# Performance work log

Hardware: AMD Instinct MI355X
Metric: run time of the kernel (lower is better)

## Reference

```python
import jax, jax.numpy as jnp
import numpy as np
import math

B, T, D_MODEL, N_HEADS = 4, 2048, 1024, 16
D_HEAD = D_MODEL // N_HEADS


def _rope_freqs(t, d_head):
    inv = 1.0 / (10000.0 ** (np.arange(0, d_head, 2, dtype=np.float32) / d_head))
    ang = np.arange(t, dtype=np.float32)[:, None] * inv[None, :]  # (T, d_head//2)
    return jnp.asarray(np.cos(ang)), jnp.asarray(np.sin(ang))


def setup_inputs() -> dict:
    key = jax.random.key(0)
    k1, k2, k3, k4, k5 = jax.random.split(key, 5)
    s = 1.0 / math.sqrt(D_MODEL)
    x = jax.random.normal(k1, (B, T, D_MODEL), dtype=jnp.float32)
    mask = jnp.triu(jnp.ones((T, T), dtype=bool), k=1)  # causal: mask future positions
    freqs_cos, freqs_sin = _rope_freqs(T, D_HEAD)
    qkv_w = jax.random.uniform(k2, (3 * D_MODEL, D_MODEL), jnp.float32, -s, s)
    qkv_b = jax.random.uniform(k3, (3 * D_MODEL,), jnp.float32, -s, s)
    proj_w = jax.random.uniform(k4, (D_MODEL, D_MODEL), jnp.float32, -s, s)
    proj_b = jax.random.uniform(k5, (D_MODEL,), jnp.float32, -s, s)
    return {"x": x, "mask": mask, "freqs_cos": freqs_cos, "freqs_sin": freqs_sin,
            "qkv_w": qkv_w, "qkv_b": qkv_b, "proj_w": proj_w, "proj_b": proj_b}


def _apply_rope(t, cos, sin):
    # t: (B, H, T, D_HEAD); cos/sin: (T, D_HEAD//2), broadcast over B, H
    tp = t.reshape(*t.shape[:-1], -1, 2)
    a, b = tp[..., 0], tp[..., 1]
    out_r = a * cos - b * sin
    out_i = a * sin + b * cos
    return jnp.stack([out_r, out_i], axis=-1).reshape(t.shape)


def reference(x, mask, freqs_cos, freqs_sin, qkv_w, qkv_b, proj_w, proj_b):
    Bx, Tx, C = x.shape
    qkv = x @ qkv_w.T + qkv_b  # (B, T, 3C)
    q, k, v = jnp.split(qkv, 3, axis=-1)
    def heads(z):
        return z.reshape(Bx, Tx, N_HEADS, D_HEAD).transpose(0, 2, 1, 3)  # (B,H,T,dh)
    q, k, v = heads(q), heads(k), heads(v)
    q = _apply_rope(q, freqs_cos, freqs_sin)
    k = _apply_rope(k, freqs_cos, freqs_sin)
    att = jnp.einsum('bhqd,bhkd->bhqk', q, k) / math.sqrt(D_HEAD)
    att = jnp.where(mask, -jnp.inf, att)
    att = jax.nn.softmax(att, axis=-1)
    out = jnp.einsum('bhqk,bhkd->bhqd', att, v)
    out = out.transpose(0, 2, 1, 3).reshape(Bx, Tx, C)
    return out @ proj_w.T + proj_b
```

## Files before the change

### kernel.cpp

```cpp
#include <hip/hip_runtime.h>
#include <stdint.h>

#define BB 4
#define TT 2048
#define CC 1024
#define HH 16
#define DH 64
#define NQKV 3072

typedef __bf16 bf16_t;
typedef __attribute__((ext_vector_type(8))) __bf16 bf16x8;
typedef __attribute__((ext_vector_type(4))) float f32x4;

#define MFMA16(a, b, c) __builtin_amdgcn_mfma_f32_16x16x32_bf16((a), (b), (c), 0, 0, 0)

__device__ __forceinline__ void gll16(const void* g, void* l) {
  typedef const __attribute__((address_space(1))) void* gp_t;
  typedef __attribute__((address_space(3))) void* lp_t;
  __builtin_amdgcn_global_load_lds((gp_t)(uintptr_t)g, (lp_t)(uintptr_t)l, 16, 0, 0);
}

__global__ __launch_bounds__(256) void cvt_k(const float* __restrict__ src,
                                             bf16_t* __restrict__ dst, int n) {
  const int i8 = (blockIdx.x * 256 + threadIdx.x) * 8;
  if (i8 < n) {
    const f32x4 a = *(const f32x4*)(src + i8);
    const f32x4 b = *(const f32x4*)(src + i8 + 4);
    bf16x8 r;
    r[0] = (bf16_t)a[0]; r[1] = (bf16_t)a[1]; r[2] = (bf16_t)a[2]; r[3] = (bf16_t)a[3];
    r[4] = (bf16_t)b[0]; r[5] = (bf16_t)b[1]; r[6] = (bf16_t)b[2]; r[7] = (bf16_t)b[3];
    *(bf16x8*)(dst + i8) = r;
  }
}

template <int EPI>
__global__ __launch_bounds__(512, 2) void gemm_k(
    const bf16_t* __restrict__ A, const bf16_t* __restrict__ W,
    const float* __restrict__ bias,
    const float* __restrict__ fcos, const float* __restrict__ fsin,
    void* __restrict__ out0v, bf16_t* __restrict__ out1,
    bf16_t* __restrict__ out2) {
  __shared__ bf16_t Al[2][16384];
  __shared__ bf16_t Bl[2][16384];
  const int K = 1024;
  const int tid = threadIdx.x;
  const int lane = tid & 63, wave = tid >> 6;
  const int quad = lane >> 4, c = lane & 15;
  const int wm = wave >> 2, wn = wave & 3;
  const int mbase = blockIdx.y * 256, nbase = blockIdx.x * 256;

  f32x4 acc[8][4];
#pragma unroll
  for (int i = 0; i < 8; ++i)
#pragma unroll
    for (int j = 0; j < 4; ++j) acc[i][j] = (f32x4){0.f, 0.f, 0.f, 0.f};

  const int r0 = tid >> 3;
  const int cc0 = (tid & 7) ^ (r0 & 7);
  const bf16_t* Ag = A + (size_t)(mbase + r0) * K + cc0 * 8;
  const bf16_t* Bg = W + (size_t)(nbase + r0) * K + cc0 * 8;
  const int ls0 = tid * 8, ls1 = ls0 + 4096, ls2 = ls0 + 8192, ls3 = ls0 + 12288;

  const int rbA = (wm * 128 + c) * 64;
  const int rbB = (wn * 64 + c) * 64;
  const int sw0 = (quad ^ (c & 7)) * 8;

#define STAGE(CUR, T)                                  \
  {                                                    \
    const int ko_ = (T)*64;                            \
    gll16(Ag + ko_, &Al[CUR][ls0]);                    \
    gll16(Ag + 64 * K + ko_, &Al[CUR][ls1]);           \
    gll16(Ag + 128 * K + ko_, &Al[CUR][ls2]);          \
    gll16(Ag + 192 * K + ko_, &Al[CUR][ls3]);          \
    gll16(Bg + ko_, &Bl[CUR][ls0]);                    \
    gll16(Bg + 64 * K + ko_, &Bl[CUR][ls1]);           \
    gll16(Bg + 128 * K + ko_, &Bl[CUR][ls2]);          \
    gll16(Bg + 192 * K + ko_, &Bl[CUR][ls3]);          \
  }

#define KTILE(T, CUR, VM, DOSTAGE)                                            \
  {                                                                           \
    asm volatile("s_waitcnt vmcnt(" #VM ")" ::: "memory");                    \
    __builtin_amdgcn_s_barrier();                                             \
    asm volatile("" ::: "memory");                                            \
    bf16x8 af0[8], bf0[4], af1[8], bf1[4];                                    \
    _Pragma("unroll") for (int mi = 0; mi < 8; ++mi)                          \
        af0[mi] = *(const bf16x8*)&Al[CUR][rbA + mi * 1024 + sw0];            \
    _Pragma("unroll") for (int ni = 0; ni < 4; ++ni)                          \
        bf0[ni] = *(const bf16x8*)&Bl[CUR][rbB + ni * 1024 + sw0];            \
    __builtin_amdgcn_s_setprio(1);                                            \
    _Pragma("unroll") for (int mi = 0; mi < 8; ++mi)                          \
        _Pragma("unroll") for (int ni = 0; ni < 4; ++ni)                      \
            acc[mi][ni] = MFMA16(af0[mi], bf0[ni], acc[mi][ni]);              \
    __builtin_amdgcn_s_setprio(0);                                            \
    _Pragma("unroll") for (int mi = 0; mi < 8; ++mi)                          \
        af1[mi] = *(const bf16x8*)&Al[CUR][rbA + mi * 1024 + (sw0 ^ 32)];     \
    _Pragma("unroll") for (int ni = 0; ni < 4; ++ni)                          \
        bf1[ni] = *(const bf16x8*)&Bl[CUR][rbB + ni * 1024 + (sw0 ^ 32)];     \
    asm volatile("s_waitcnt lgkmcnt(0)" ::: "memory");                        \
    __builtin_amdgcn_s_barrier();   \
    asm volatile("" ::: "memory");                                            \
    if (DOSTAGE) STAGE(CUR, (T) + 2);                                         \
    __builtin_amdgcn_s_setprio(1);                                            \
    _Pragma("unroll") for (int mi = 0; mi < 8; ++mi)                          \
        _Pragma("unroll") for (int ni = 0; ni < 4; ++ni)                      \
            acc[mi][ni] = MFMA16(af1[mi], bf1[ni], acc[mi][ni]);              \
    __builtin_amdgcn_s_setprio(0);                                            \
  }

  STAGE(0, 0);
  STAGE(1, 1);

  for (int fj = 0; fj < 7; ++fj) {
    const int t0 = 2 * fj;
    KTILE(t0, 0, 8, 1)
    KTILE(t0 + 1, 1, 8, 1)
  }
  KTILE(14, 0, 8, 0)
  KTILE(15, 1, 0, 0)
#undef KTILE
#undef STAGE

  const float qscale = 0.18033688011112042f;
#pragma unroll
  for (int mi = 0; mi < 8; ++mi) {
#pragma unroll
    for (int ni = 0; ni < 4; ++ni) {
      const int n = nbase + wn * 64 + ni * 16 + c;
      const float bv = bias[n];
#pragma unroll
      for (int r = 0; r < 4; ++r) {
        const int m = mbase + wm * 128 + mi * 16 + quad * 4 + r;
        float v = acc[mi][ni][r] + bv;
        if (EPI == 0) {
          bf16_t* out0 = (bf16_t*)out0v;
          const int sel = n >> 10;
          const int nl = n & 1023;
          const int h = nl >> 6, d = nl & 63;
          const int b = m >> 11, t = m & 2047;
          const int dst = ((b * HH + h) * TT + t) * DH + d;
          if (sel < 2) {
            const float pv = __shfl_xor(v, 1, 64);
            const int d2 = d >> 1;
            const float cs = fcos[t * 32 + d2];
            const float sn = fsin[t * 32 + d2];
            float o = ((d & 1) == 0) ? (v * cs - pv * sn) : (pv * sn + v * cs);
            if (sel == 0) {
              o *= qscale;
              out0[dst] = (bf16_t)o;
            } else {
              out1[dst] = (bf16_t)o;
            }
          } else {
            out2[dst] = (bf16_t)v;
          }
        } else {
          float* outf = (float*)out0v;
          outf[(size_t)m * CC + n] = v;
        }
      }
    }
  }
}

__global__ __launch_bounds__(256, 4) void attn_k(const bf16_t* __restrict__ Q,
                                                 const bf16_t* __restrict__ Kv,
                                                 const bf16_t* __restrict__ V,
                                                 bf16_t* __restrict__ O) {
  __shared__ bf16_t KS[2][64 * 64];
  __shared__ bf16_t VtS[2][64 * 64];
  __shared__ bf16_t PS[4][16 * 64];

  const int tid = threadIdx.x;
  const int lane = tid & 63, wave = tid >> 6;
  const int quad = lane >> 4, c = lane & 15;
  const int bi = blockIdx.x;
  const int pair = bi & 15, h = (bi >> 4) & 15, b = bi >> 8;
  const int qtA = pair, qtB = 31 - pair;
  const int nA = qtA + 1;

  const bf16_t* Qh = Q + ((b * HH + h) * TT) * DH;
  const bf16_t* Kh = Kv + ((b * HH + h) * TT) * DH;
  const bf16_t* Vh = V + ((b * HH + h) * TT) * DH;

  const f32x4 zero4 = {0.f, 0.f, 0.f, 0.f};
  bf16x8 ones8;
#pragma unroll
  for (int i = 0; i < 8; ++i) ones8[i] = (bf16_t)1.0f;

  const int krow0 = tid >> 3, kc8 = tid & 7, krow1 = krow0 + 32;
  const bf16_t* kbase0 = Kh + krow0 * DH + kc8 * 8;
  const bf16_t* kbase1 = Kh + krow1 * DH + kc8 * 8;
  const int vsb = tid >> 2, vjp = tid & 3;
  const int vrg = vsb & 7, vc8 = vsb >> 3;
  const int vd0 = vc8 * 8 + vjp * 2, vd1 = vd0 + 1;
  const bf16_t* vbase = Vh + vrg * 8 * DH + vd0;

  const int sw = c & 7;
  const int e0 = c * 64 + (quad ^ sw) * 8;
  const int e1 = c * 64 + ((quad + 4) ^ sw) * 8;

  bf16x8 kr0, kr1;
  uint32_t vr[8];
  auto load_tile = [&](int eoff) {
    kr0 = *(const bf16x8*)(kbase0 + eoff);
    kr1 = *(const bf16x8*)(kbase1 + eoff);
    const bf16_t* vp = vbase + eoff;
#pragma unroll
    for (int i = 0; i < 8; ++i) vr[i] = *(const uint32_t*)(vp + i * DH);
  };
  auto store_tile = [&](int buf) {
    *(bf16x8*)&KS[buf][(krow0 * 8 + (kc8 ^ (krow0 & 7))) * 8] = kr0;
    *(bf16x8*)&KS[buf][(krow1 * 8 + (kc8 ^ (krow1 & 7))) * 8] = kr1;
    union { bf16x8 v; uint16_t u[8]; } colA, colB;
#pragma unroll
    for (int i = 0; i < 8; ++i) {
      colA.u[i] = (uint16_t)(vr[i] & 0xffffu);
      colB.u[i] = (uint16_t)(vr[i] >> 16);
    }
    *(bf16x8*)&VtS[buf][(vd0 * 8 + (vrg ^ (vd0 & 7))) * 8] = colA.v;
    *(bf16x8*)&VtS[buf][(vd1 * 8 + (vrg ^ (vd1 & 7))) * 8] = colB.v;
  };

  int qtbase = qtA * 64;
  bf16x8 qf0 = *(const bf16x8*)(Qh + (qtbase + wave * 16 + c) * DH + quad * 8);
  bf16x8 qf1 = *(const bf16x8*)(Qh + (qtbase + wave * 16 + c) * DH + 32 + quad * 8);

  f32x4 o_acc[4] = {zero4, zero4, zero4, zero4};
  float m_r[4] = {-1e30f, -1e30f, -1e30f, -1e30f};
  float l_r[4] = {0.f, 0.f, 0.f, 0.f};

  auto write_O = [&](int qtb) {
#pragma unroll
    for (int r = 0; r < 4; ++r) {
      const int qg = qtb + wave * 16 + quad * 4 + r;
      const float inv = 1.0f / l_r[r];
#pragma unroll
      for (int ni = 0; ni < 4; ++ni)
        O[(b * TT + qg) * CC + h * 64 + ni * 16 + c] =
            (bf16_t)(o_acc[ni][r] * inv);
    }
  };

  load_tile(0);
  store_tile(0);
  __syncthreads();
  int coff = 0;
  int kkey = 0;

#define ATTN_ITER(FI, CUR)                                                     \
  {                                                                            \
    const int fi_ = (FI);                                                      \
    const bool pre_ = fi_ < 32;                                                \
    const int noff_ = (fi_ + 1 == nA) ? 0 : coff + 64 * DH;                    \
    if (pre_) load_tile(noff_);                                                \
    bf16x8 kf0[4], kf1[4];                                                     \
    _Pragma("unroll") for (int ni = 0; ni < 4; ++ni) {                         \
      kf0[ni] = *(const bf16x8*)&KS[CUR][ni * 1024 + e0];                      \
      kf1[ni] = *(const bf16x8*)&KS[CUR][ni * 1024 + e1];                      \
    }                                                                          \
    f32x4 s[4];                                                                \
    _Pragma("unroll") for (int ni = 0; ni < 4; ++ni) {                         \
      f32x4 t = MFMA16(qf0, kf0[ni], zero4);                                   \
      t = MFMA16(qf1, kf1[ni], t);                                             \
      s[ni] = t;                                                               \
    }                                                                          \
    const int minq_ = qtbase + wave * 16;                                      \
    if (kkey + 63 > minq_) {                                                   \
      _Pragma("unroll") for (int ni = 0; ni < 4; ++ni)                         \
          _Pragma("unroll") for (int r = 0; r < 4; ++r) {                      \
        const int key_ = kkey + ni * 16 + c;                                   \
        const int qg_ = minq_ + quad * 4 + r;                                  \
        if (key_ > qg_) s[ni][r] = -1e30f;                                     \
      }                                                                        \
    }                                                                          \
    float alpha[4];                                                            \
    _Pragma("unroll") for (int r = 0; r < 4; ++r) {                            \
      float mx = fmaxf(fmaxf(s[0][r], s[1][r]), fmaxf(s[2][r], s[3][r]));      \
      mx = fmaxf(mx, __shfl_xor(mx, 1, 64));                                   \
      mx = fmaxf(mx, __shfl_xor(mx, 2, 64));                                   \
      mx = fmaxf(mx, __shfl_xor(mx, 4, 64));                                   \
      mx = fmaxf(mx, __shfl_xor(mx, 8, 64));                                   \
      const float mnew = fmaxf(m_r[r], mx);                                    \
      alpha[r] = __builtin_amdgcn_exp2f(m_r[r] - mnew);                        \
      m_r[r] = mnew;                                                           \
    }                                                                          \
    _Pragma("unroll") for (int ni = 0; ni < 4; ++ni)                           \
        _Pragma("unroll") for (int r = 0; r < 4; ++r) {                        \
      const float p = __builtin_amdgcn_exp2f(s[ni][r] - m_r[r]);               \
      const int prow_ = quad * 4 + r, pcol_ = ni * 16 + c;                     \
      PS[wave][(prow_ * 8 + ((pcol_ >> 3) ^ (prow_ & 7))) * 8 + (pcol_ & 7)] = \
          (bf16_t)p;                                                           \
    }                                                                          \
    _Pragma("unroll") for (int r = 0; r < 4; ++r) {                            \
      _Pragma("unroll") for (int ni = 0; ni < 4; ++ni)                         \
          o_acc[ni][r] *= alpha[r];                                            \
    }                                                                          \
    asm volatile("s_waitcnt lgkmcnt(0)" ::: "memory");                         \
    const bf16x8 p0 = *(const bf16x8*)&PS[wave][e0];                           \
    const bf16x8 p1 = *(const bf16x8*)&PS[wave][e1];                           \
    f32x4 rs = MFMA16(p0, ones8, zero4);                                       \
    rs = MFMA16(p1, ones8, rs);                                                \
    _Pragma("unroll") for (int ni = 0; ni < 4; ++ni) {                         \
      const bf16x8 v0 = *(const bf16x8*)&VtS[CUR][ni * 1024 + e0];             \
      const bf16x8 v1 = *(const bf16x8*)&VtS[CUR][ni * 1024 + e1];             \
      o_acc[ni] = MFMA16(p0, v0, o_acc[ni]);                                   \
      o_acc[ni] = MFMA16(p1, v1, o_acc[ni]);                                   \
    }                                                                          \
    _Pragma("unroll") for (int r = 0; r < 4; ++r)                              \
        l_r[r] = l_r[r] * alpha[r] + rs[r];                                    \
    if (fi_ == nA - 1) {                                                       \
      write_O(qtbase);                                                         \
      qtbase = qtB * 64;                                                       \
      qf0 = *(const bf16x8*)(Qh + (qtbase + wave * 16 + c) * DH + quad * 8);   \
      qf1 = *(const bf16x8*)(Qh + (qtbase + wave * 16 + c) * DH + 32 +         \
                             quad * 8);                                        \
      _Pragma("unroll") for (int r = 0; r < 4; ++r) {                          \
        m_r[r] = -1e30f;                                                       \
        l_r[r] = 0.f;                                                          \
      }                                                                        \
      _Pragma("unroll") for (int ni = 0; ni < 4; ++ni) o_acc[ni] = zero4;      \
    }                                                                          \
    if (pre_) store_tile(1 - (CUR));                                           \
    __syncthreads();                                                           \
    coff = noff_;                                                              \
    kkey = (fi_ + 1 == nA) ? 0 : kkey + 64;                                    \
  }

  for (int fj = 0; fj < 16; ++fj) {
    ATTN_ITER(2 * fj, 0)
    ATTN_ITER(2 * fj + 1, 1)
  }
  ATTN_ITER(32, 0)
#undef ATTN_ITER

  write_O(qtbase);
}

extern "C" void kernel_launch(void* const* d_in, const int* in_sizes, int n_in,
                              void* d_out, int out_size, void* d_ws,
                              size_t ws_size, hipStream_t stream) {
  const float *x = nullptr, *fcos = nullptr, *fsin = nullptr;
  const float *qkv_w = nullptr, *qkv_b = nullptr, *proj_w = nullptr, *proj_b = nullptr;
  for (int i = 0; i < n_in; ++i) {
    const int s = in_sizes[i];
    const float* p = (const float*)d_in[i];
    if (s == BB * TT * CC) x = p;
    else if (s == TT * (DH / 2)) { if (!fcos) fcos = p; else fsin = p; }
    else if (s == NQKV * CC) qkv_w = p;
    else if (s == NQKV) qkv_b = p;
    else if (s == CC * CC) proj_w = p;
    else if (s == CC) proj_b = p;
  }

  const size_t NE = (size_t)BB * TT * CC;
  bf16_t* Qb = (bf16_t*)d_ws;
  bf16_t* Kb = Qb + NE;
  bf16_t* Vb = Kb + NE;
  bf16_t* Ob = Vb + NE;
  bf16_t* xb = Ob;
  bf16_t* wqkvb = (bf16_t*)d_out;
  bf16_t* wpb = Qb;

  cvt_k<<<dim3((int)(NE / 2048)), 256, 0, stream>>>(x, xb, (int)NE);
  cvt_k<<<dim3(NQKV * CC / 2048), 256, 0, stream>>>(qkv_w, wqkvb, NQKV * CC);

  gemm_k<0><<<dim3(NQKV / 256, (BB * TT) / 256), 512, 0, stream>>>(
      xb, wqkvb, qkv_b, fcos, fsin, (void*)Qb, Kb, Vb);
  attn_k<<<dim3(BB * HH * 16), 256, 0, stream>>>(Qb, Kb, Vb, Ob);
  cvt_k<<<dim3(CC * CC / 2048), 256, 0, stream>>>(proj_w, wpb, CC * CC);
  gemm_k<1><<<dim3(CC / 256, (BB * TT) / 256), 512, 0, stream>>>(
      Ob, wpb, proj_b, nullptr, nullptr, d_out, nullptr, nullptr);
}
```

Baseline: 339.8 us.

## Split GEMM K-tiles into half-tile LDS stages with finer-grained prefetch

Restructures the bf16 GEMM main loop so that A and B tiles are staged in half-K sub-buffers, and global-to-LDS loads for the next tiles are interleaved between four MFMA sub-phases. The intent is better overlap of memory loads with matrix math. The output-projection GEMM also gets a templated narrower N tile (128 instead of 256), which doubles its grid so more CUs are busy. In exchange there are more barriers per K-tile and more complex vmcnt bookkeeping, which risks correctness or extra stalls.

```diff
diff --git a/kernel.cpp b/kernel.cpp
--- a/kernel.cpp
+++ b/kernel.cpp
@@ -19,6 +19,21 @@
   typedef __attribute__((address_space(3))) void* lp_t;
   __builtin_amdgcn_global_load_lds((gp_t)(uintptr_t)g, (lp_t)(uintptr_t)l, 16, 0, 0);
 }
+
+template <int N>
+__device__ __forceinline__ void vmwait() {
+  if constexpr (N == 0) asm volatile("s_waitcnt vmcnt(0)" ::: "memory");
+  else if constexpr (N == 2) asm volatile("s_waitcnt vmcnt(2)" ::: "memory");
+  else if constexpr (N == 6) asm volatile("s_waitcnt vmcnt(6)" ::: "memory");
+  else if constexpr (N == 8) asm volatile("s_waitcnt vmcnt(8)" ::: "memory");
+}
+
+#define LGKM0                                          \
+  do {                                                 \
+    asm volatile("s_waitcnt lgkmcnt(0)" ::: "memory"); \
+    __builtin_amdgcn_sched_barrier(0);                 \
+  } while (0)
+#define BAR() __builtin_amdgcn_s_barrier()
 
 __global__ __launch_bounds__(256) void cvt_k(const float* __restrict__ src,
                                              bf16_t* __restrict__ dst, int n) {
@@ -33,100 +48,153 @@
   }
 }
 
-template <int EPI>
+template <int EPI, int NI>
 __global__ __launch_bounds__(512, 2) void gemm_k(
     const bf16_t* __restrict__ A, const bf16_t* __restrict__ W,
     const float* __restrict__ bias,
     const float* __restrict__ fcos, const float* __restrict__ fsin,
     void* __restrict__ out0v, bf16_t* __restrict__ out1,
     bf16_t* __restrict__ out2) {
-  __shared__ bf16_t Al[2][16384];
-  __shared__ bf16_t Bl[2][16384];
+  constexpr int BN = NI * 64;
+  __shared__ bf16_t Al[2][2][8192];
+  __shared__ bf16_t Bl[2][2][BN * 32];
   const int K = 1024;
   const int tid = threadIdx.x;
-  const int lane = tid & 63, wave = tid >> 6;
-  const int quad = lane >> 4, c = lane & 15;
+  const int wave = tid >> 6;
+  const int quad = (tid & 63) >> 4, c = tid & 15;
   const int wm = wave >> 2, wn = wave & 3;
-  const int mbase = blockIdx.y * 256, nbase = blockIdx.x * 256;
-
-  f32x4 acc[8][4];
+  const int mbase = blockIdx.y * 256, nbase = blockIdx.x * BN;
+
+  f32x4 acc[8][NI];
 #pragma unroll
   for (int i = 0; i < 8; ++i)
 #pragma unroll
-    for (int j = 0; j < 4; ++j) acc[i][j] = (f32x4){0.f, 0.f, 0.f, 0.f};
-
-  const int r0 = tid >> 3;
-  const int cc0 = (tid & 7) ^ (r0 & 7);
-  const bf16_t* Ag = A + (size_t)(mbase + r0) * K + cc0 * 8;
-  const bf16_t* Bg = W + (size_t)(nbase + r0) * K + cc0 * 8;
-  const int ls0 = tid * 8, ls1 = ls0 + 4096, ls2 = ls0 + 8192, ls3 = ls0 + 12288;
-
-  const int rbA = (wm * 128 + c) * 64;
-  const int rbB = (wn * 64 + c) * 64;
-  const int sw0 = (quad ^ (c & 7)) * 8;
-
-#define STAGE(CUR, T)                                  \
-  {                                                    \
-    const int ko_ = (T)*64;                            \
-    gll16(Ag + ko_, &Al[CUR][ls0]);                    \
-    gll16(Ag + 64 * K + ko_, &Al[CUR][ls1]);           \
-    gll16(Ag + 128 * K + ko_, &Al[CUR][ls2]);          \
-    gll16(Ag + 192 * K + ko_, &Al[CUR][ls3]);          \
-    gll16(Bg + ko_, &Bl[CUR][ls0]);                    \
-    gll16(Bg + 64 * K + ko_, &Bl[CUR][ls1]);           \
-    gll16(Bg + 128 * K + ko_, &Bl[CUR][ls2]);          \
-    gll16(Bg + 192 * K + ko_, &Bl[CUR][ls3]);          \
-  }
-
-#define KTILE(T, CUR, VM, DOSTAGE)                                            \
+    for (int j = 0; j < NI; ++j) acc[i][j] = (f32x4){0.f, 0.f, 0.f, 0.f};
+
+  const int base_r = wm * 64 + c;
+  const int swA0 = (quad ^ (c & 7)) * 8;
+  const int rbB = (wn * (NI * 16) + c) * 32;
+  const int swB = (quad ^ ((c >> 1) & 3)) * 8;
+
+  const int sr = tid >> 3;
+  const int saq = ((tid & 7) ^ (sr & 7)) * 8;
+  const bf16_t* aS0 = A + (size_t)(mbase + sr) * K + saq;
+  const bf16_t* aS1 = A + (size_t)(mbase + 64 + sr) * K + saq;
+  const int br = tid >> 2;
+  const int sbq = ((tid & 3) ^ ((tid >> 3) & 3)) * 8;
+  const bf16_t* bS0 = W + (size_t)(nbase + br) * K + sbq;
+  const bf16_t* bS1 = bS0 + 32;
+
+#define STAGE_A0(BUF, KT)                                                \
+  {                                                                      \
+    gll16(aS0 + (KT)*64, &Al[BUF][0][tid * 8]);                          \
+    gll16(aS0 + 128 * K + (KT)*64, &Al[BUF][0][tid * 8 + 4096]);         \
+  }
+#define STAGE_A1(BUF, KT)                                                \
+  {                                                                      \
+    gll16(aS1 + (KT)*64, &Al[BUF][1][tid * 8]);                          \
+    gll16(aS1 + 128 * K + (KT)*64, &Al[BUF][1][tid * 8 + 4096]);         \
+  }
+#define STAGE_B0(BUF, KT)                                                \
+  {                                                                      \
+    gll16(bS0 + (KT)*64, &Bl[BUF][0][tid * 8]);                          \
+    if constexpr (NI == 4)                                               \
+      gll16(bS0 + 128 * K + (KT)*64, &Bl[BUF][0][tid * 8 + 4096]);       \
+  }
+#define STAGE_B1(BUF, KT)                                                \
+  {                                                                      \
+    gll16(bS1 + (KT)*64, &Bl[BUF][1][tid * 8]);                          \
+    if constexpr (NI == 4)                                               \
+      gll16(bS1 + 128 * K + (KT)*64, &Bl[BUF][1][tid * 8 + 4096]);       \
+  }
+
+  constexpr int WS = (NI == 4) ? 8 : 6;
+
+#define KTILE(BUF, W2, WN, S1, S2, S4, KT)                                    \
   {                                                                           \
-    asm volatile("s_waitcnt vmcnt(" #VM ")" ::: "memory");                    \
-    __builtin_amdgcn_s_barrier();                                             \
-    asm volatile("" ::: "memory");                                            \
-    bf16x8 af0[8], bf0[4], af1[8], bf1[4];                                    \
-    _Pragma("unroll") for (int mi = 0; mi < 8; ++mi)                          \
-        af0[mi] = *(const bf16x8*)&Al[CUR][rbA + mi * 1024 + sw0];            \
-    _Pragma("unroll") for (int ni = 0; ni < 4; ++ni)                          \
-        bf0[ni] = *(const bf16x8*)&Bl[CUR][rbB + ni * 1024 + sw0];            \
+    const int kt_ = (KT);                                                     \
+    bf16x8 a_[4], b_[NI];                                                     \
+                                                     \
+    _Pragma("unroll") for (int i = 0; i < 4; ++i)                             \
+        a_[i] = *(const bf16x8*)&Al[BUF][0][(base_r + i * 16) * 64 + swA0];   \
+    _Pragma("unroll") for (int i = 0; i < NI; ++i)                            \
+        b_[i] = *(const bf16x8*)&Bl[BUF][0][rbB + i * 512 + swB];             \
+    if (S1) STAGE_A1((BUF) ^ 1, kt_ + 1);                                     \
+    BAR();                                                                    \
+    LGKM0;                                                                    \
     __builtin_amdgcn_s_setprio(1);                                            \
-    _Pragma("unroll") for (int mi = 0; mi < 8; ++mi)                          \
-        _Pragma("unroll") for (int ni = 0; ni < 4; ++ni)                      \
-            acc[mi][ni] = MFMA16(af0[mi], bf0[ni], acc[mi][ni]);              \
+    _Pragma("unroll") for (int mi = 0; mi < 4; ++mi)                          \
+        _Pragma("unroll") for (int ni = 0; ni < NI; ++ni)                     \
+            acc[mi][ni] = MFMA16(a_[mi], b_[ni], acc[mi][ni]);                \
     __builtin_amdgcn_s_setprio(0);                                            \
-    _Pragma("unroll") for (int mi = 0; mi < 8; ++mi)                          \
-        af1[mi] = *(const bf16x8*)&Al[CUR][rbA + mi * 1024 + (sw0 ^ 32)];     \
-    _Pragma("unroll") for (int ni = 0; ni < 4; ++ni)                          \
-        bf1[ni] = *(const bf16x8*)&Bl[CUR][rbB + ni * 1024 + (sw0 ^ 32)];     \
-    asm volatile("s_waitcnt lgkmcnt(0)" ::: "memory");                        \
-    __builtin_amdgcn_s_barrier();   \
-    asm volatile("" ::: "memory");                                            \
-    if (DOSTAGE) STAGE(CUR, (T) + 2);                                         \
+    vmwait<W2>();                                                             \
+    BAR();                                                                    \
+                                                     \
+    _Pragma("unroll") for (int i = 0; i < 4; ++i)                             \
+        a_[i] = *(const bf16x8*)&Al[BUF][1][(base_r + i * 16) * 64 + swA0];   \
+    if (S2) STAGE_B0(BUF, kt_ + 2);                                           \
+    BAR();                                                                    \
+    LGKM0;                                                                    \
     __builtin_amdgcn_s_setprio(1);                                            \
-    _Pragma("unroll") for (int mi = 0; mi < 8; ++mi)                          \
-        _Pragma("unroll") for (int ni = 0; ni < 4; ++ni)                      \
-            acc[mi][ni] = MFMA16(af1[mi], bf1[ni], acc[mi][ni]);              \
+    _Pragma("unroll") for (int mi = 0; mi < 4; ++mi)                          \
+        _Pragma("unroll") for (int ni = 0; ni < NI; ++ni)                     \
+            acc[4 + mi][ni] = MFMA16(a_[mi], b_[ni], acc[4 + mi][ni]);        \
     __builtin_amdgcn_s_setprio(0);                                            \
-  }
-
-  STAGE(0, 0);
-  STAGE(1, 1);
+    BAR();                                                                    \
+                                                     \
+    _Pragma("unroll") for (int i = 0; i < 4; ++i)                             \
+        a_[i] = *(const bf16x8*)&Al[BUF][0]                                   \
+                    [(base_r + i * 16) * 64 + (swA0 ^ 32)];                   \
+    _Pragma("unroll") for (int i = 0; i < NI; ++i)                            \
+        b_[i] = *(const bf16x8*)&Bl[BUF][1][rbB + i * 512 + swB];             \
+    BAR();                                                                    \
+    LGKM0;                                                                    \
+    __builtin_amdgcn_s_setprio(1);                                            \
+    _Pragma("unroll") for (int mi = 0; mi < 4; ++mi)                          \
+        _Pragma("unroll") for (int ni = 0; ni < NI; ++ni)                     \
+            acc[mi][ni] = MFMA16(a_[mi], b_[ni], acc[mi][ni]);                \
+    __builtin_amdgcn_s_setprio(0);                                            \
+    BAR();                                                                    \
+                                                     \
+    _Pragma("unroll") for (int i = 0; i < 4; ++i)                             \
+        a_[i] = *(const bf16x8*)&Al[BUF][1]                                   \
+                    [(base_r + i * 16) * 64 + (swA0 ^ 32)];                   \
+    if (S4) { STAGE_B1(BUF, kt_ + 2); STAGE_A0(BUF, kt_ + 2); }               \
+    BAR();                                                                    \
+    LGKM0;                                                                    \
+    __builtin_amdgcn_s_setprio(1);                                            \
+    _Pragma("unroll") for (int mi = 0; mi < 4; ++mi)                          \
+        _Pragma("unroll") for (int ni = 0; ni < NI; ++ni)                     \
+            acc[4 + mi][ni] = MFMA16(a_[mi], b_[ni], acc[4 + mi][ni]);        \
+    __builtin_amdgcn_s_setprio(0);                                            \
+    vmwait<WN>();                                                             \
+    BAR();                                                                    \
+  }
+
+  STAGE_B0(0, 0); STAGE_B1(0, 0); STAGE_A0(0, 0); STAGE_A1(0, 0);
+  STAGE_B0(1, 1); STAGE_B1(1, 1); STAGE_A0(1, 1);
+  vmwait<WS>();
+  BAR();
 
   for (int fj = 0; fj < 7; ++fj) {
     const int t0 = 2 * fj;
-    KTILE(t0, 0, 8, 1)
-    KTILE(t0 + 1, 1, 8, 1)
-  }
-  KTILE(14, 0, 8, 0)
-  KTILE(15, 1, 0, 0)
+    KTILE(0, WS, WS, 1, 1, 1, t0)
+    KTILE(1, WS, WS, 1, 1, 1, t0 + 1)
+  }
+  KTILE(0, WS, 2, 1, 0, 0, 14)
+  KTILE(1, 0, 0, 0, 0, 0, 15)
 #undef KTILE
-#undef STAGE
+#undef STAGE_A0
+#undef STAGE_A1
+#undef STAGE_B0
+#undef STAGE_B1
 
   const float qscale = 0.18033688011112042f;
 #pragma unroll
   for (int mi = 0; mi < 8; ++mi) {
 #pragma unroll
-    for (int ni = 0; ni < 4; ++ni) {
-      const int n = nbase + wn * 64 + ni * 16 + c;
+    for (int ni = 0; ni < NI; ++ni) {
+      const int n = nbase + wn * (NI * 16) + ni * 16 + c;
       const float bv = bias[n];
 #pragma unroll
       for (int r = 0; r < 4; ++r) {
@@ -365,10 +433,10 @@
   cvt_k<<<dim3((int)(NE / 2048)), 256, 0, stream>>>(x, xb, (int)NE);
   cvt_k<<<dim3(NQKV * CC / 2048), 256, 0, stream>>>(qkv_w, wqkvb, NQKV * CC);
 
-  gemm_k<0><<<dim3(NQKV / 256, (BB * TT) / 256), 512, 0, stream>>>(
+  gemm_k<0, 4><<<dim3(NQKV / 256, (BB * TT) / 256), 512, 0, stream>>>(
       xb, wqkvb, qkv_b, fcos, fsin, (void*)Qb, Kb, Vb);
   attn_k<<<dim3(BB * HH * 16), 256, 0, stream>>>(Qb, Kb, Vb, Ob);
   cvt_k<<<dim3(CC * CC / 2048), 256, 0, stream>>>(proj_w, wpb, CC * CC);
-  gemm_k<1><<<dim3(CC / 256, (BB * TT) / 256), 512, 0, stream>>>(
+  gemm_k<1, 2><<<dim3(CC / 128, (BB * TT) / 256), 512, 0, stream>>>(
       Ob, wpb, proj_b, nullptr, nullptr, d_out, nullptr, nullptr);
 }
```

Result: no change. 335.1 us (-1.4%).
